# Kernel optimization log

Hardware: AMD Instinct MI355X
Metric: run time of the kernel (lower is better)

The kernel has to match this reference:

```python
import jax, jax.numpy as jnp
import numpy as np

DIM0, DIMO, WIDTH, DEPTH = 64, 16, 128, 6  # depth = number of weight matrices
N = 524288


def setup_inputs() -> dict:
    key = jax.random.key(0)
    ks = jax.random.split(key, DEPTH + 1)
    x = jax.random.normal(ks[0], (N, DIM0), dtype=jnp.float32)
    bd0 = 1.0 / np.sqrt(DIM0)   # first layer init bound (per torch code)
    bd = 1.0 / np.sqrt(WIDTH)   # remaining layers init bound
    W0 = jax.random.uniform(ks[1], (DIM0, WIDTH), minval=-bd0, maxval=bd0, dtype=jnp.float32)
    W1 = jax.random.uniform(ks[2], (WIDTH, WIDTH), minval=-bd, maxval=bd, dtype=jnp.float32)
    W2 = jax.random.uniform(ks[3], (WIDTH, WIDTH), minval=-bd, maxval=bd, dtype=jnp.float32)
    W3 = jax.random.uniform(ks[4], (WIDTH, WIDTH), minval=-bd, maxval=bd, dtype=jnp.float32)
    W4 = jax.random.uniform(ks[5], (WIDTH, WIDTH), minval=-bd, maxval=bd, dtype=jnp.float32)
    W5 = jax.random.uniform(ks[6], (WIDTH, DIMO), minval=-bd, maxval=bd, dtype=jnp.float32)
    bias = jnp.zeros((DIMO,), dtype=jnp.float32)
    return {"x": x, "W0": W0, "W1": W1, "W2": W2, "W3": W3, "W4": W4, "W5": W5, "bias": bias}


def reference(x, W0, W1, W2, W3, W4, W5, bias):
    # Fully-fused MLP math: matmul (no bias) + ReLU for every layer except the
    # last (output_activation='None'); then cast back to x dtype and add bias.
    h = jax.nn.relu(x @ W0)
    h = jax.nn.relu(h @ W1)
    h = jax.nn.relu(h @ W2)
    h = jax.nn.relu(h @ W3)
    h = jax.nn.relu(h @ W4)
    out = (h @ W5).astype(x.dtype) + bias
    return out
```

## Files before the change

kernel.cpp:

```cpp
#include <hip/hip_runtime.h>
#include <stdint.h>


typedef __bf16 bf16x8 __attribute__((ext_vector_type(8)));
typedef __bf16 bf16x4 __attribute__((ext_vector_type(4)));
typedef float  floatx4  __attribute__((ext_vector_type(4)));
typedef float  floatx16 __attribute__((ext_vector_type(16)));

constexpr int NS   = 524288;
constexpr int SPW  = 64;
constexpr int WPB  = 4;
constexpr int TILE = SPW * WPB;
constexpr int NBLK = NS / TILE;

constexpr int WTOT = 9728;

__global__ void prep_weights(const float* __restrict__ W0, const float* __restrict__ W1,
                             const float* __restrict__ W2, const float* __restrict__ W3,
                             const float* __restrict__ W4, const float* __restrict__ W5,
                             bf16x8* __restrict__ ws) {
  int gid = blockIdx.x * blockDim.x + threadIdx.x;
  if (gid >= WTOT) return;
  const float* Wsrc; int nout, MT, base;
  if (gid < 1024)      { Wsrc = W0; nout = 128; MT = 4; base = 0;    }
  else if (gid < 3072) { Wsrc = W1; nout = 128; MT = 4; base = 1024; }
  else if (gid < 5120) { Wsrc = W2; nout = 128; MT = 4; base = 3072; }
  else if (gid < 7168) { Wsrc = W3; nout = 128; MT = 4; base = 5120; }
  else if (gid < 9216) { Wsrc = W4; nout = 128; MT = 4; base = 7168; }
  else                 { Wsrc = W5; nout = 16;  MT = 1; base = 9216; }
  int id  = gid - base;
  int l   = id & 63, blk = id >> 6;
  int mt  = blk % MT, ks = blk / MT;
  int row = mt * 32 + (l & 31);
  int k0  = ks * 16 + (l >> 5) * 8;
  bf16x8 v;
#pragma unroll
  for (int j = 0; j < 8; ++j)
    v[j] = (row < nout) ? (__bf16)Wsrc[(k0 + j) * nout + row] : (__bf16)0.0f;
  ws[gid] = v;
}

__device__ __forceinline__ bf16x8 h_read(const bf16x8* Hw, int nt, int ks, int n31, int h) {
  int c = 2 * ks + h;
  int row = nt * 32 + n31;
  return Hw[row * 16 + (c ^ (n31 & 7))];
}

template <int KS>
__device__ __forceinline__ void layer_mm(const bf16x8* __restrict__ wg,
                                         const bf16x8* Hw, floatx16 acc[2][4],
                                         int l, int n31, int h) {
  bf16x8 a_cur[4], b_cur[2];
#pragma unroll
  for (int mt = 0; mt < 4; ++mt) a_cur[mt] = wg[mt * 64 + l];
  b_cur[0] = h_read(Hw, 0, 0, n31, h);
  b_cur[1] = h_read(Hw, 1, 0, n31, h);
#pragma unroll
  for (int ks = 0; ks < KS; ++ks) {
    bf16x8 a_nxt[4], b_nxt[2];
    if (ks + 1 < KS) {
#pragma unroll
      for (int mt = 0; mt < 4; ++mt) a_nxt[mt] = wg[((ks + 1) * 4 + mt) * 64 + l];
      b_nxt[0] = h_read(Hw, 0, ks + 1, n31, h);
      b_nxt[1] = h_read(Hw, 1, ks + 1, n31, h);
    }
#pragma unroll
    for (int nt = 0; nt < 2; ++nt)
#pragma unroll
      for (int mt = 0; mt < 4; ++mt)
        acc[nt][mt] = __builtin_amdgcn_mfma_f32_32x32x16_bf16(a_cur[mt], b_cur[nt], acc[nt][mt], 0, 0, 0);
    if (ks + 1 < KS) {
#pragma unroll
      for (int mt = 0; mt < 4; ++mt) a_cur[mt] = a_nxt[mt];
      b_cur[0] = b_nxt[0]; b_cur[1] = b_nxt[1];
    }
  }
}

__device__ __forceinline__ void zero_acc(floatx16 acc[2][4]) {
#pragma unroll
  for (int nt = 0; nt < 2; ++nt)
#pragma unroll
    for (int mt = 0; mt < 4; ++mt)
#pragma unroll
      for (int r = 0; r < 16; ++r) acc[nt][mt][r] = 0.0f;
}

__device__ __forceinline__ void write_h(bf16x4* H8, const floatx16 acc[2][4],
                                        int n31, int h) {
#pragma unroll
  for (int nt = 0; nt < 2; ++nt) {
    int row_s = nt * 32 + n31;
#pragma unroll
    for (int mt = 0; mt < 4; ++mt)
#pragma unroll
      for (int q = 0; q < 4; ++q) {
        bf16x4 v;
#pragma unroll
        for (int j = 0; j < 4; ++j) v[j] = (__bf16)fmaxf(acc[nt][mt][4 * q + j], 0.0f);
        int c = 4 * mt + q;
        H8[row_s * 32 + (c ^ (n31 & 7)) * 2 + h] = v;
      }
  }
}

__global__ void __launch_bounds__(256, 2) mlp_kernel(const float* __restrict__ x,
                                                     const float* __restrict__ bias,
                                                     const bf16x8* __restrict__ wimg,
                                                     float* __restrict__ out) {
  __shared__ bf16x8 Hbuf[WPB * 64 * 16];

  const int t   = threadIdx.x;
  const int l   = t & 63;
  const int w   = t >> 6;
  const int n31 = l & 31;
  const int h   = l >> 5;
  bf16x8* Hw = Hbuf + w * (64 * 16);
  const size_t S0 = (size_t)blockIdx.x * TILE + (size_t)w * SPW;

  const float* xw = x + S0 * 64;
#pragma unroll
  for (int it = 0; it < 8; ++it) {
    int id = it * 64 + l, s = id >> 3, c = id & 7;
    const floatx4* p = (const floatx4*)(xw + id * 8);
    floatx4 lo = p[0], hi = p[1];
    bf16x8 v;
    v[0] = (__bf16)lo[0]; v[1] = (__bf16)lo[1]; v[2] = (__bf16)lo[2]; v[3] = (__bf16)lo[3];
    v[4] = (__bf16)hi[0]; v[5] = (__bf16)hi[1]; v[6] = (__bf16)hi[2]; v[7] = (__bf16)hi[3];
    Hw[s * 16 + (c ^ (s & 7))] = v;
  }

  floatx16 acc[2][4];

  zero_acc(acc);
  layer_mm<4>(wimg, Hw, acc, l, n31, h);
  write_h((bf16x4*)Hw, acc, n31, h);

  constexpr int WOFF[4] = {1024, 3072, 5120, 7168};
#pragma unroll
  for (int ly = 0; ly < 4; ++ly) {
    zero_acc(acc);
    layer_mm<8>(wimg + WOFF[ly], Hw, acc, l, n31, h);
    write_h((bf16x4*)Hw, acc, n31, h);
  }

  floatx16 a5[2];
#pragma unroll
  for (int nt = 0; nt < 2; ++nt)
#pragma unroll
    for (int r = 0; r < 16; ++r) a5[nt][r] = 0.0f;

  {
    const bf16x8* wg5 = wimg + 9216;
    bf16x8 a_cur = wg5[l];
    bf16x8 b_cur[2] = {h_read(Hw, 0, 0, n31, h), h_read(Hw, 1, 0, n31, h)};
#pragma unroll
    for (int ks = 0; ks < 8; ++ks) {
      bf16x8 a_nxt; bf16x8 b_nxt[2];
      if (ks + 1 < 8) {
        a_nxt = wg5[(ks + 1) * 64 + l];
        b_nxt[0] = h_read(Hw, 0, ks + 1, n31, h);
        b_nxt[1] = h_read(Hw, 1, ks + 1, n31, h);
      }
      a5[0] = __builtin_amdgcn_mfma_f32_32x32x16_bf16(a_cur, b_cur[0], a5[0], 0, 0, 0);
      a5[1] = __builtin_amdgcn_mfma_f32_32x32x16_bf16(a_cur, b_cur[1], a5[1], 0, 0, 0);
      if (ks + 1 < 8) { a_cur = a_nxt; b_cur[0] = b_nxt[0]; b_cur[1] = b_nxt[1]; }
    }
  }

  floatx4 bv0 = *(const floatx4*)(bias + 4 * h);
  floatx4 bv1 = *(const floatx4*)(bias + 8 + 4 * h);
  floatx4* outv = (floatx4*)out;
#pragma unroll
  for (int nt = 0; nt < 2; ++nt) {
    size_t s = S0 + nt * 32 + n31;
    floatx4 o0, o1;
#pragma unroll
    for (int j = 0; j < 4; ++j) { o0[j] = a5[nt][j] + bv0[j]; o1[j] = a5[nt][4 + j] + bv1[j]; }
    outv[s * 4 + h]     = o0;
    outv[s * 4 + 2 + h] = o1;
  }
}

extern "C" void kernel_launch(void* const* d_in, const int* in_sizes, int n_in,
                              void* d_out, int out_size, void* d_ws, size_t ws_size,
                              hipStream_t stream) {
  (void)in_sizes; (void)n_in; (void)out_size; (void)ws_size;
  const float* x    = (const float*)d_in[0];
  const float* W0   = (const float*)d_in[1];
  const float* W1   = (const float*)d_in[2];
  const float* W2   = (const float*)d_in[3];
  const float* W3   = (const float*)d_in[4];
  const float* W4   = (const float*)d_in[5];
  const float* W5   = (const float*)d_in[6];
  const float* bias = (const float*)d_in[7];
  bf16x8* ws = (bf16x8*)d_ws;

  prep_weights<<<(WTOT + 255) / 256, 256, 0, stream>>>(W0, W1, W2, W3, W4, W5, ws);
  mlp_kernel<<<NBLK, 256, 0, stream>>>(x, bias, (const bf16x8*)ws, (float*)d_out);
}
```

Before: 280.1 us.

## Keep MLP activations in registers via cross-half shuffles instead of LDS

Drops the per-wave LDS activation buffer. Each layer's MFMA accumulator output is converted to bf16 after ReLU and rearranged into the next layer's B-operand layout with __shfl_xor across the two 32-lane halves, so activations stay in VGPRs. Weight fragments are double-buffered, and the first k-slice of the next layer's weights is prefetched during the last step of the current layer. Input x is loaded straight into B registers. This removes LDS write and read traffic between layers but holds 16 bf16x8 B fragments in registers, which may raise VGPR pressure and threaten the 2-blocks-per-CU launch bound.

```diff
diff --git a/kernel.cpp b/kernel.cpp
--- a/kernel.cpp
+++ b/kernel.cpp
@@ -40,40 +40,29 @@
   ws[gid] = v;
 }
 
-__device__ __forceinline__ bf16x8 h_read(const bf16x8* Hw, int nt, int ks, int n31, int h) {
-  int c = 2 * ks + h;
-  int row = nt * 32 + n31;
-  return Hw[row * 16 + (c ^ (n31 & 7))];
-}
+union Q8 { bf16x4 v; int u[2]; };
 
-template <int KS>
-__device__ __forceinline__ void layer_mm(const bf16x8* __restrict__ wg,
-                                         const bf16x8* Hw, floatx16 acc[2][4],
-                                         int l, int n31, int h) {
-  bf16x8 a_cur[4], b_cur[2];
+__device__ __forceinline__ void tile_to_b(const floatx16 v, bf16x8 b[],
+                                          int mt, int h, bf16x8* bdst_nt ) {
+  bf16x4 quad[4];
 #pragma unroll
-  for (int mt = 0; mt < 4; ++mt) a_cur[mt] = wg[mt * 64 + l];
-  b_cur[0] = h_read(Hw, 0, 0, n31, h);
-  b_cur[1] = h_read(Hw, 1, 0, n31, h);
+  for (int q = 0; q < 4; ++q)
 #pragma unroll
-  for (int ks = 0; ks < KS; ++ks) {
-    bf16x8 a_nxt[4], b_nxt[2];
-    if (ks + 1 < KS) {
+    for (int i = 0; i < 4; ++i)
+      quad[q][i] = (__bf16)fmaxf(v[4 * q + i], 0.0f);
 #pragma unroll
-      for (int mt = 0; mt < 4; ++mt) a_nxt[mt] = wg[((ks + 1) * 4 + mt) * 64 + l];
-      b_nxt[0] = h_read(Hw, 0, ks + 1, n31, h);
-      b_nxt[1] = h_read(Hw, 1, ks + 1, n31, h);
-    }
+  for (int qp = 0; qp < 2; ++qp) {
+    bf16x4 keep = h ? quad[2 * qp + 1] : quad[2 * qp];
+    Q8 s; s.v = h ? quad[2 * qp] : quad[2 * qp + 1];
+    Q8 r;
+    r.u[0] = __shfl_xor(s.u[0], 32, 64);
+    r.u[1] = __shfl_xor(s.u[1], 32, 64);
+    bf16x4 low  = h ? r.v : keep;
+    bf16x4 high = h ? keep : r.v;
+    bf16x8 bb;
 #pragma unroll
-    for (int nt = 0; nt < 2; ++nt)
-#pragma unroll
-      for (int mt = 0; mt < 4; ++mt)
-        acc[nt][mt] = __builtin_amdgcn_mfma_f32_32x32x16_bf16(a_cur[mt], b_cur[nt], acc[nt][mt], 0, 0, 0);
-    if (ks + 1 < KS) {
-#pragma unroll
-      for (int mt = 0; mt < 4; ++mt) a_cur[mt] = a_nxt[mt];
-      b_cur[0] = b_nxt[0]; b_cur[1] = b_nxt[1];
-    }
+    for (int i = 0; i < 4; ++i) { bb[i] = low[i]; bb[4 + i] = high[i]; }
+    bdst_nt[2 * mt + qp] = bb;
   }
 }
 
@@ -86,86 +75,95 @@
       for (int r = 0; r < 16; ++r) acc[nt][mt][r] = 0.0f;
 }
 
-__device__ __forceinline__ void write_h(bf16x4* H8, const floatx16 acc[2][4],
-                                        int n31, int h) {
+template <int KS>
+__device__ __forceinline__ void layer_mm(const bf16x8* __restrict__ wg,
+                                         const bf16x8* __restrict__ wg_next,
+                                         bf16x8 a[2][4], const bf16x8 b[2][8],
+                                         floatx16 acc[2][4], int l) {
 #pragma unroll
-  for (int nt = 0; nt < 2; ++nt) {
-    int row_s = nt * 32 + n31;
+  for (int ks = 0; ks < KS; ++ks) {
+    const int cur = ks & 1, nxt = cur ^ 1;
+    if (ks + 1 < KS) {
+#pragma unroll
+      for (int mt = 0; mt < 4; ++mt) a[nxt][mt] = wg[((ks + 1) * 4 + mt) * 64 + l];
+    } else {
+#pragma unroll
+      for (int mt = 0; mt < 4; ++mt) a[nxt][mt] = wg_next[mt * 64 + l];
+    }
+#pragma unroll
+    for (int nt = 0; nt < 2; ++nt)
+#pragma unroll
+      for (int mt = 0; mt < 4; ++mt)
+        acc[nt][mt] = __builtin_amdgcn_mfma_f32_32x32x16_bf16(a[cur][mt], b[nt][ks],
+                                                              acc[nt][mt], 0, 0, 0);
+  }
+}
+
+__device__ __forceinline__ void epilogue_to_b(const floatx16 acc[2][4], bf16x8 b[2][8],
+                                              int h) {
+#pragma unroll
+  for (int nt = 0; nt < 2; ++nt)
 #pragma unroll
     for (int mt = 0; mt < 4; ++mt)
-#pragma unroll
-      for (int q = 0; q < 4; ++q) {
-        bf16x4 v;
-#pragma unroll
-        for (int j = 0; j < 4; ++j) v[j] = (__bf16)fmaxf(acc[nt][mt][4 * q + j], 0.0f);
-        int c = 4 * mt + q;
-        H8[row_s * 32 + (c ^ (n31 & 7)) * 2 + h] = v;
-      }
-  }
+      tile_to_b(acc[nt][mt], nullptr, mt, h, &b[nt][0]);
 }
 
 __global__ void __launch_bounds__(256, 2) mlp_kernel(const float* __restrict__ x,
                                                      const float* __restrict__ bias,
                                                      const bf16x8* __restrict__ wimg,
                                                      float* __restrict__ out) {
-  __shared__ bf16x8 Hbuf[WPB * 64 * 16];
-
   const int t   = threadIdx.x;
   const int l   = t & 63;
   const int w   = t >> 6;
   const int n31 = l & 31;
   const int h   = l >> 5;
-  bf16x8* Hw = Hbuf + w * (64 * 16);
   const size_t S0 = (size_t)blockIdx.x * TILE + (size_t)w * SPW;
+
+  bf16x8 a[2][4];
+  bf16x8 b[2][8];
+  floatx16 acc[2][4];
+
+#pragma unroll
+  for (int mt = 0; mt < 4; ++mt) a[0][mt] = wimg[mt * 64 + l];
 
   const float* xw = x + S0 * 64;
 #pragma unroll
-  for (int it = 0; it < 8; ++it) {
-    int id = it * 64 + l, s = id >> 3, c = id & 7;
-    const floatx4* p = (const floatx4*)(xw + id * 8);
-    floatx4 lo = p[0], hi = p[1];
-    bf16x8 v;
-    v[0] = (__bf16)lo[0]; v[1] = (__bf16)lo[1]; v[2] = (__bf16)lo[2]; v[3] = (__bf16)lo[3];
-    v[4] = (__bf16)hi[0]; v[5] = (__bf16)hi[1]; v[6] = (__bf16)hi[2]; v[7] = (__bf16)hi[3];
-    Hw[s * 16 + (c ^ (s & 7))] = v;
-  }
-
-  floatx16 acc[2][4];
+  for (int nt = 0; nt < 2; ++nt)
+#pragma unroll
+    for (int ks = 0; ks < 4; ++ks) {
+      const floatx4* p = (const floatx4*)(xw + (nt * 32 + n31) * 64 + ks * 16 + h * 8);
+      floatx4 lo = p[0], hi = p[1];
+      bf16x8 v;
+#pragma unroll
+      for (int i = 0; i < 4; ++i) { v[i] = (__bf16)lo[i]; v[4 + i] = (__bf16)hi[i]; }
+      b[nt][ks] = v;
+    }
 
   zero_acc(acc);
-  layer_mm<4>(wimg, Hw, acc, l, n31, h);
-  write_h((bf16x4*)Hw, acc, n31, h);
+  layer_mm<4>(wimg, wimg + 1024, a, b, acc, l);
+  epilogue_to_b(acc, b, h);
 
-  constexpr int WOFF[4] = {1024, 3072, 5120, 7168};
+  constexpr int WOFF[5] = {1024, 3072, 5120, 7168, 9216};
 #pragma unroll
   for (int ly = 0; ly < 4; ++ly) {
     zero_acc(acc);
-    layer_mm<8>(wimg + WOFF[ly], Hw, acc, l, n31, h);
-    write_h((bf16x4*)Hw, acc, n31, h);
+    layer_mm<8>(wimg + WOFF[ly], wimg + WOFF[ly + 1], a, b, acc, l);
+    epilogue_to_b(acc, b, h);
   }
 
+#pragma unroll
+  for (int mt = 0; mt < 4; ++mt) a[1][mt] = wimg[9216 + (4 + mt) * 64 + l];
   floatx16 a5[2];
 #pragma unroll
   for (int nt = 0; nt < 2; ++nt)
 #pragma unroll
     for (int r = 0; r < 16; ++r) a5[nt][r] = 0.0f;
-
-  {
-    const bf16x8* wg5 = wimg + 9216;
-    bf16x8 a_cur = wg5[l];
-    bf16x8 b_cur[2] = {h_read(Hw, 0, 0, n31, h), h_read(Hw, 1, 0, n31, h)};
 #pragma unroll
-    for (int ks = 0; ks < 8; ++ks) {
-      bf16x8 a_nxt; bf16x8 b_nxt[2];
-      if (ks + 1 < 8) {
-        a_nxt = wg5[(ks + 1) * 64 + l];
-        b_nxt[0] = h_read(Hw, 0, ks + 1, n31, h);
-        b_nxt[1] = h_read(Hw, 1, ks + 1, n31, h);
-      }
-      a5[0] = __builtin_amdgcn_mfma_f32_32x32x16_bf16(a_cur, b_cur[0], a5[0], 0, 0, 0);
-      a5[1] = __builtin_amdgcn_mfma_f32_32x32x16_bf16(a_cur, b_cur[1], a5[1], 0, 0, 0);
-      if (ks + 1 < 8) { a_cur = a_nxt; b_cur[0] = b_nxt[0]; b_cur[1] = b_nxt[1]; }
-    }
+  for (int ks = 0; ks < 8; ++ks) {
+    bf16x8 f = a[ks >> 2][ks & 3];
+#pragma unroll
+    for (int nt = 0; nt < 2; ++nt)
+      a5[nt] = __builtin_amdgcn_mfma_f32_32x32x16_bf16(f, b[nt][ks], a5[nt], 0, 0, 0);
   }
 
   floatx4 bv0 = *(const floatx4*)(bias + 4 * h);
```

Result: faster. 270.2 us (-3.6%).
